# Optimization experiments

Hardware: AMD Instinct MI355X
Metric: run time of the kernel (lower is better)

## Reference

```python
import jax, jax.numpy as jnp
import numpy as np

L = 10   # lattice side (hardcoded self.length)
K = 3    # kernel_size -> half_k = 1 wrap padding
FN = 4   # filter_num
B = 262144


def setup_inputs() -> dict:
    key = jax.random.key(0)
    k1, k2, k3, k4, k5 = jax.random.split(key, 5)
    v = jax.random.normal(k1, (B, L * L), dtype=jnp.float32)
    # torch default init scale ~ 1/sqrt(fan_in)
    conv_w = jax.random.normal(k2, (FN, 1, K, K), dtype=jnp.float32) / 3.0
    conv_b = jax.random.normal(k3, (FN,), dtype=jnp.float32) * 0.1
    deconv_w = jax.random.normal(k4, (FN, 1, 2, 2), dtype=jnp.float32) / 4.0
    deconv_b = jax.random.normal(k5, (1,), dtype=jnp.float32) * 0.1
    data = jnp.zeros((1,), dtype=jnp.int32)  # unused positional arg of log_psi
    return {"v": v, "conv_w": conv_w, "conv_b": conv_b,
            "deconv_w": deconv_w, "deconv_b": deconv_b, "data": data}


def _log_psi(v, conv_w, conv_b, deconv_w, deconv_b):
    b = v.shape[0]
    x = v.reshape(b, 1, L, L)
    # handmade_padding == periodic (wrap) pad of width half_k=1 on both spatial axes
    x = jnp.pad(x, ((0, 0), (0, 0), (1, 1), (1, 1)), mode="wrap")  # [B,1,12,12]
    # Conv2d(1, FN, 3), VALID -> [B,FN,10,10]
    y = jax.lax.conv_general_dilated(
        x, conv_w, window_strides=(1, 1), padding="VALID",
        dimension_numbers=("NCHW", "OIHW", "NCHW"))
    y = y + conv_b[None, :, None, None]
    # MaxPool2d(2,2): non-overlapping 2x2 -> [B,FN,5,5]
    y = y.reshape(b, FN, L // 2, 2, L // 2, 2).max(axis=(3, 5))
    # ConvTranspose2d(FN,1,kernel=2,stride=2): each input pixel -> disjoint 2x2 block
    # torch weight layout [in=FN, out=1, 2, 2]
    z = jnp.einsum("bcij,cokl->boikjl", y, deconv_w).reshape(b, 1, L, L)
    z = z + deconv_b[None, :, None, None]
    sign_z = jnp.sign(z)
    abs_z = z * sign_z
    sign_prod = sign_z.reshape(b, -1).prod(axis=1)        # scalar per sample
    log_sum = jnp.log(abs_z).reshape(b, -1).sum(axis=1)   # scalar per sample
    return sign_prod, log_sum


def reference(v, conv_w, conv_b, deconv_w, deconv_b, data):
    return _log_psi(v, conv_w, conv_b, deconv_w, deconv_b)
```

## Files before the change

kernel.cpp:

```cpp
#include <hip/hip_runtime.h>
#include <math.h>


typedef float v2f __attribute__((ext_vector_type(2)));

#define SREAD(x) __int_as_float(__builtin_amdgcn_readfirstlane(__float_as_int(x)))
#define WAITVM(N) asm volatile("s_waitcnt vmcnt(" #N ")" ::: "memory")
#define WAITLGKM0() asm volatile("s_waitcnt lgkmcnt(0)" ::: "memory")
#define MEMFENCE() asm volatile("" ::: "memory")

__device__ __forceinline__ float dpp_swap1_f(float x) {
    return __int_as_float(__builtin_amdgcn_mov_dpp(__float_as_int(x), 0xB1, 0xF, 0xF, true));
}
__device__ __forceinline__ float dpp_swap2_f(float x) {
    return __int_as_float(__builtin_amdgcn_mov_dpp(__float_as_int(x), 0x4E, 0xF, 0xF, true));
}
__device__ __forceinline__ unsigned dpp_swap1_u(unsigned x) {
    return (unsigned)__builtin_amdgcn_mov_dpp((int)x, 0xB1, 0xF, 0xF, true);
}
__device__ __forceinline__ unsigned dpp_swap2_u(unsigned x) {
    return (unsigned)__builtin_amdgcn_mov_dpp((int)x, 0x4E, 0xF, 0xF, true);
}

__device__ __forceinline__ void gload16(const float* g, float* l) {
    __builtin_amdgcn_global_load_lds(
        (const __attribute__((address_space(1))) void*)g,
        (__attribute__((address_space(3))) void*)l, 16, 0, 0);
}
__device__ __forceinline__ void gload4(const float* g, float* l) {
    __builtin_amdgcn_global_load_lds(
        (const __attribute__((address_space(1))) void*)g,
        (__attribute__((address_space(3))) void*)l, 4, 0, 0);
}

__global__ __launch_bounds__(128, 3) void CNN2D_37495064494620_kernel(
    const float* __restrict__ v,
    const float* __restrict__ cw,
    const float* __restrict__ cb,
    const float* __restrict__ dw,
    const float* __restrict__ db,
    float* __restrict__ out,
    int B)
{
    const int lane = threadIdx.x & 63;
    const int w    = threadIdx.x >> 6;
    const int q    = lane & 1;
    const int h    = (lane >> 1) & 1;
    const int g    = lane >> 2;

    __shared__ __align__(16) float smraw[6400];
    float* sm = smraw + w * 3200;

    float Wf[4][9];
    #pragma unroll
    for (int f = 0; f < 4; ++f)
        #pragma unroll
        for (int t = 0; t < 9; ++t)
            Wf[f][t] = SREAD(cw[f * 9 + t]);
    v2f Wsel[9];
    #pragma unroll
    for (int t = 0; t < 9; ++t)
        Wsel[t] = (v2f){ h ? Wf[2][t] : Wf[0][t], h ? Wf[3][t] : Wf[1][t] };
    const float cb0 = SREAD(cb[0]), cb1 = SREAD(cb[1]);
    const float cb2 = SREAD(cb[2]), cb3 = SREAD(cb[3]);
    const v2f Cbsel = (v2f){ h ? cb2 : cb0, h ? cb3 : cb1 };

    float Dw4[4][4];
    #pragma unroll
    for (int f = 0; f < 4; ++f)
        #pragma unroll
        for (int t = 0; t < 4; ++t)
            Dw4[f][t] = SREAD(dw[f * 4 + t]);
    const float Db = SREAD(db[0]);
    float Dkl[4];
    #pragma unroll
    for (int f = 0; f < 4; ++f) {
        const float e01 = h ? Dw4[f][1] : Dw4[f][0];
        const float e23 = h ? Dw4[f][3] : Dw4[f][2];
        Dkl[f] = q ? e23 : e01;
    }
    const float Ds0 = h ? Dkl[2] : Dkl[0];
    const float Ds1 = h ? Dkl[3] : Dkl[1];
    const float Ds2 = h ? Dkl[0] : Dkl[2];
    const float Ds3 = h ? Dkl[1] : Dkl[3];

    WAITVM(0);

    const float* gbase = v + (size_t)blockIdx.x * 12800 + w * 6400;

    auto STAGE = [&](int b) {
        const float* gb = gbase + b * 1600;
        float* lb = sm + (b & 1) * 1600;
        #pragma unroll
        for (int k = 0; k < 6; ++k)
            gload16(gb + k * 256 + lane * 4, lb + k * 256);
        gload4(gb + 1536 + lane, lb + 1536);
    };

    STAGE(0);
    MEMFENCE();
    STAGE(1);

    #pragma unroll 1
    for (int b = 0; b < 4; ++b) {
        if (b < 3) WAITVM(7); else WAITVM(0);

        const float* my = sm + (b & 1) * 1600 + g * 100;
        unsigned sb = 0u;
        float l2 = 0.0f;

        #pragma unroll
        for (int i = 0; i < 5; ++i) {
            const int r1 = 2 * i + q;
            const int r0 = (i == 0) ? (q ? 0 : 9) : (2 * i - 1 + q);
            const int r2 = (i == 4) ? (q ? 0 : 9) : (2 * i + 1 + q);

            float R[3][10];
            #pragma unroll
            for (int t = 0; t < 5; ++t) {
                float2 x0 = *(const float2*)(my + r0 * 10 + 2 * t);
                float2 x1 = *(const float2*)(my + r1 * 10 + 2 * t);
                float2 x2 = *(const float2*)(my + r2 * 10 + 2 * t);
                R[0][2 * t] = x0.x; R[0][2 * t + 1] = x0.y;
                R[1][2 * t] = x1.x; R[1][2 * t + 1] = x1.y;
                R[2][2 * t] = x2.x; R[2][2 * t + 1] = x2.y;
            }

            #pragma unroll
            for (int j = 0; j < 5; ++j) {
                v2f a0 = Cbsel, a1 = Cbsel;
                #pragma unroll
                for (int kr = 0; kr < 3; ++kr) {
                    #pragma unroll
                    for (int kc = 0; kc < 3; ++kc) {
                        const int cc0 = (2 * j + kc + 9) % 10;
                        const int cc1 = (2 * j + 1 + kc + 9) % 10;
                        const int t = kr * 3 + kc;
                        const v2f x0 = (v2f){R[kr][cc0], R[kr][cc0]};
                        const v2f x1 = (v2f){R[kr][cc1], R[kr][cc1]};
                        a0 = __builtin_elementwise_fma(x0, Wsel[t], a0);
                        a1 = __builtin_elementwise_fma(x1, Wsel[t], a1);
                    }
                }
                const v2f m = __builtin_elementwise_max(a0, a1);
                const float Px = fmaxf(m.x, dpp_swap1_f(m.x));
                const float Py = fmaxf(m.y, dpp_swap1_f(m.y));
                const float Qx = dpp_swap2_f(Px);
                const float Qy = dpp_swap2_f(Py);
                float z = Db;
                z = fmaf(Px, Ds0, z);
                z = fmaf(Py, Ds1, z);
                z = fmaf(Qx, Ds2, z);
                z = fmaf(Qy, Ds3, z);
                sb ^= __float_as_uint(z);
                l2 += __log2f(fabsf(z));
            }
        }

        l2 += dpp_swap1_f(l2);
        l2 += dpp_swap2_f(l2);
        sb ^= dpp_swap1_u(sb);
        sb ^= dpp_swap2_u(sb);

        const int s = blockIdx.x * 128 + w * 64 + b * 16 + g;
        const int r = lane & 3;
        if (r == 0)      out[s]     = (sb & 0x80000000u) ? -1.0f : 1.0f;
        else if (r == 1) out[B + s] = l2 * 0.69314718055994531f;

        if (b < 2) { WAITLGKM0(); STAGE(b + 2); }
    }
}

extern "C" void kernel_launch(void* const* d_in, const int* in_sizes, int n_in,
                              void* d_out, int out_size, void* d_ws, size_t ws_size,
                              hipStream_t stream) {
    const float* v  = (const float*)d_in[0];
    const float* cw = (const float*)d_in[1];
    const float* cb = (const float*)d_in[2];
    const float* dw = (const float*)d_in[3];
    const float* db = (const float*)d_in[4];
    float* out = (float*)d_out;

    const int B = in_sizes[0] / 100;
    const int grid = B / 128;
    CNN2D_37495064494620_kernel<<<grid, 128, 0, stream>>>(v, cw, cb, dw, db, out, B);
}
```

Before: 180.6 us.

## Use single-wave blocks with two-stage loads and pair log products

Each block is now one wave that handles 32 samples: it issues both LDS stages up front and computes them in turn, replacing the persistent 4-iteration ring loop of two-wave blocks. This gives many more, smaller blocks, removing the loop's LDS reuse waits in favour of latency hiding across waves. Separately, adjacent z values are multiplied in pairs before log2, roughly halving the number of log evaluations. Taking the product risks underflow or overflow in rare cases.

```diff
diff --git a/kernel.cpp b/kernel.cpp
--- a/kernel.cpp
+++ b/kernel.cpp
@@ -6,7 +6,6 @@
 
 #define SREAD(x) __int_as_float(__builtin_amdgcn_readfirstlane(__float_as_int(x)))
 #define WAITVM(N) asm volatile("s_waitcnt vmcnt(" #N ")" ::: "memory")
-#define WAITLGKM0() asm volatile("s_waitcnt lgkmcnt(0)" ::: "memory")
 #define MEMFENCE() asm volatile("" ::: "memory")
 
 __device__ __forceinline__ float dpp_swap1_f(float x) {
@@ -33,7 +32,7 @@
         (__attribute__((address_space(3))) void*)l, 4, 0, 0);
 }
 
-__global__ __launch_bounds__(128, 3) void CNN2D_37495064494620_kernel(
+__global__ __launch_bounds__(64, 4) void CNN2D_37495064494620_kernel(
     const float* __restrict__ v,
     const float* __restrict__ cw,
     const float* __restrict__ cb,
@@ -42,14 +41,12 @@
     float* __restrict__ out,
     int B)
 {
-    const int lane = threadIdx.x & 63;
-    const int w    = threadIdx.x >> 6;
+    const int lane = threadIdx.x;
     const int q    = lane & 1;
     const int h    = (lane >> 1) & 1;
     const int g    = lane >> 2;
 
-    __shared__ __align__(16) float smraw[6400];
-    float* sm = smraw + w * 3200;
+    __shared__ __align__(16) float sm[3200];
 
     float Wf[4][9];
     #pragma unroll
@@ -86,28 +83,22 @@
 
     WAITVM(0);
 
-    const float* gbase = v + (size_t)blockIdx.x * 12800 + w * 6400;
+    const float* gbase = v + (size_t)blockIdx.x * 3200;
 
     auto STAGE = [&](int b) {
         const float* gb = gbase + b * 1600;
-        float* lb = sm + (b & 1) * 1600;
+        float* lb = sm + b * 1600;
         #pragma unroll
         for (int k = 0; k < 6; ++k)
             gload16(gb + k * 256 + lane * 4, lb + k * 256);
         gload4(gb + 1536 + lane, lb + 1536);
     };
 
-    STAGE(0);
-    MEMFENCE();
-    STAGE(1);
-
-    #pragma unroll 1
-    for (int b = 0; b < 4; ++b) {
-        if (b < 3) WAITVM(7); else WAITVM(0);
-
-        const float* my = sm + (b & 1) * 1600 + g * 100;
+    auto COMPUTE = [&](const float* buf, int sbase) {
+        const float* my = buf + g * 100;
         unsigned sb = 0u;
         float l2 = 0.0f;
+        float zpend = 0.0f;
 
         #pragma unroll
         for (int i = 0; i < 5; ++i) {
@@ -152,8 +143,18 @@
                 z = fmaf(Py, Ds1, z);
                 z = fmaf(Qx, Ds2, z);
                 z = fmaf(Qy, Ds3, z);
-                sb ^= __float_as_uint(z);
-                l2 += __log2f(fabsf(z));
+
+                const int pos = i * 5 + j;
+                if (pos == 24) {
+                    sb ^= __float_as_uint(z);
+                    l2 += __log2f(fabsf(z));
+                } else if (pos & 1) {
+                    const float zp = zpend * z;
+                    sb ^= __float_as_uint(zp);
+                    l2 += __log2f(fabsf(zp));
+                } else {
+                    zpend = z;
+                }
             }
         }
 
@@ -162,13 +163,21 @@
         sb ^= dpp_swap1_u(sb);
         sb ^= dpp_swap2_u(sb);
 
-        const int s = blockIdx.x * 128 + w * 64 + b * 16 + g;
+        const int s = sbase + g;
         const int r = lane & 3;
         if (r == 0)      out[s]     = (sb & 0x80000000u) ? -1.0f : 1.0f;
         else if (r == 1) out[B + s] = l2 * 0.69314718055994531f;
+    };
 
-        if (b < 2) { WAITLGKM0(); STAGE(b + 2); }
-    }
+    STAGE(0);
+    MEMFENCE();
+    STAGE(1);
+
+    const int sb0 = blockIdx.x * 32;
+    WAITVM(7);
+    COMPUTE(sm, sb0);
+    WAITVM(0);
+    COMPUTE(sm + 1600, sb0 + 16);
 }
 
 extern "C" void kernel_launch(void* const* d_in, const int* in_sizes, int n_in,
@@ -182,6 +191,6 @@
     float* out = (float*)d_out;
 
     const int B = in_sizes[0] / 100;
-    const int grid = B / 128;
-    CNN2D_37495064494620_kernel<<<grid, 128, 0, stream>>>(v, cw, cb, dw, db, out, B);
+    const int grid = B / 32;
+    CNN2D_37495064494620_kernel<<<grid, 64, 0, stream>>>(v, cw, cb, dw, db, out, B);
 }
```

Result: faster. 169.4 us (-6.2%).
